# Kernel optimization log

Measured on AMD Instinct MI355X. Metric: run time of the kernel, lower is better.

The kernel has to match this reference:

```python
import jax, jax.numpy as jnp
import numpy as np
from jax import lax

# PRPN (Parse-Read-Predict Network), eval mode (all dropout off, BatchNorm in eval
# with running stats mean=0/var=1, rmask=ones). Submodule math follows the upstream
# yikangshen/PRPN implementation vendored by jiant: ParsingNetwork (conv gate stack,
# hard hardtanh memory gates with cumprod over slots), ReadingNetwork (masked-softmax
# attention over nslots memory + LayerNorm LSTM cell, shift-append memory update),
# PredictNetwork (attention over prediction memory, res=0 -> Linear+BN+Tanh head).

T, B, V, D, H, S, L, NL = 192, 32, 50000, 384, 384, 15, 5, 2
RES = 0.1
G4 = 4 * H
BN_SC = np.float32(1.0 / np.sqrt(1.0 + 1e-5))   # eval BatchNorm with mean=0, var=1
INV_SQRT_H = np.float32(1.0 / np.sqrt(H))


def _layer_norm(x, g, b, eps=1e-6):
    # torch-style LayerNorm with unbiased std (x.std(-1))
    mu = jnp.mean(x, -1, keepdims=True)
    var = jnp.sum((x - mu) ** 2, -1, keepdims=True) / (x.shape[-1] - 1)
    return g * (x - mu) / (jnp.sqrt(var) + eps) + b


def _msoftmax(logits, gate, eps=1e-8):
    # blocks.softmax: exp-normalize then multiply by (soft) gate mask before sum
    e = jnp.exp(logits - jnp.max(logits, -1, keepdims=True)) * gate
    return e / (jnp.sum(e, -1, keepdims=True) + eps)


def _forward(input_ids, emb_w, pconv1_w, pconv1_b, pbn_g, pbn_b, pconv2_w, pconv2_b,
             r_wih, r_bih, r_whh, r_bhh, r_lnih_g, r_lnih_b, r_lnhh_g, r_lnhh_b,
             r_lnc_g, r_lnc_b, r_proj_w, r_proj_b,
             p_proj_w, p_proj_b, p_ffd_w, p_ffd_b, p_bn_g, p_bn_b):
    emb = emb_w[input_ids]                                        # (T,B,D)

    # ---- ParsingNetwork ----
    x = jnp.concatenate([jnp.zeros((L, B, D), emb.dtype), emb], 0)  # (T+L,B,D), zero history
    xc = jnp.transpose(x, (1, 2, 0))                              # (B,D,T+L)
    h1 = lax.conv_general_dilated(xc, pconv1_w, (1,), 'VALID',
                                  dimension_numbers=('NCH', 'OIH', 'NCH'))
    h1 = h1 + pconv1_b[None, :, None]
    h1 = jax.nn.relu(pbn_g[None, :, None] * h1 * BN_SC + pbn_b[None, :, None])  # (B,H,T)
    half = H // 2
    # Conv1d(nhid, 2, 1, groups=2): channel 0 from first half, channel 1 from second
    gate = jax.nn.sigmoid(jnp.einsum('bct,c->bt', h1[:, :half], pconv2_w[0]) + pconv2_b[0])
    gate_next = jax.nn.sigmoid(jnp.einsum('bct,c->bt', h1[:, half:], pconv2_w[1]) + pconv2_b[1])
    cum = jnp.concatenate([jnp.full((B, S), 1e9, gate.dtype), gate], 1)  # init cum_gate = +inf
    gate_hat = jnp.stack([cum[:, S - k:S - k + T] for k in range(S)], 2)  # (B,T,S)

    def mem_gate(g):  # hard gates: (hardtanh((g-ghat)/res*2+1)+1)/2, cumprod over slots
        u = (jnp.clip((g[:, :, None] - gate_hat) / RES * 2.0 + 1.0, -1.0, 1.0) + 1.0) * 0.5
        return jnp.cumprod(u, axis=2)

    mg = jnp.transpose(mem_gate(gate), (1, 0, 2))                 # (T,B,S)
    mgn = jnp.transpose(mem_gate(gate_next), (1, 0, 2))           # (T,B,S)

    # ---- per-timestep Read / Predict-attention loop ----
    def step(carry, xs):
        mem_h, mem_c, pmem = carry       # (NL,B,S,H),(NL,B,S,H),(B,S,H)
        e_t, mg_t, mgn_t = xs
        h = e_t
        nh, nc = [], []
        for j in range(NL):
            mh, mc = mem_h[j], mem_c[j]
            key_j = jnp.concatenate([h, mh[:, -1]], -1) @ r_proj_w[j].T + r_proj_b[j]
            att = _msoftmax(jnp.einsum('bsh,bh->bs', mh, key_j) * INV_SQRT_H, mg_t)
            sel_h = jnp.einsum('bs,bsh->bh', att, mh)
            sel_c = jnp.einsum('bs,bsh->bh', att, mc)
            gates = (_layer_norm(h @ r_wih[j].T + r_bih[j], r_lnih_g[j], r_lnih_b[j])
                     + _layer_norm(sel_h @ r_whh[j].T + r_bhh[j], r_lnhh_g[j], r_lnhh_b[j]))
            i_g, f_g, c_g, o_g = jnp.split(gates, 4, axis=-1)
            c_new = jax.nn.sigmoid(f_g) * sel_c + jax.nn.sigmoid(i_g) * jnp.tanh(c_g)
            h_new = jax.nn.sigmoid(o_g) * jnp.tanh(_layer_norm(c_new, r_lnc_g[j], r_lnc_b[j]))
            nh.append(jnp.concatenate([mh[:, 1:], h_new[:, None]], 1))
            nc.append(jnp.concatenate([mc[:, 1:], c_new[:, None]], 1))
            h = h_new
        pkey = jnp.concatenate([h, pmem[:, -1]], -1) @ p_proj_w.T + p_proj_b
        patt = _msoftmax(jnp.einsum('bsh,bh->bs', pmem, pkey) * INV_SQRT_H, mgn_t)
        sel = jnp.einsum('bs,bsh->bh', patt, pmem)
        pmem_new = jnp.concatenate([pmem[:, 1:], h[:, None]], 1)
        return (jnp.stack(nh), jnp.stack(nc), pmem_new), (h, sel)

    carry0 = (jnp.zeros((NL, B, S, H), emb.dtype),
              jnp.zeros((NL, B, S, H), emb.dtype),
              jnp.zeros((B, S, H), emb.dtype))
    _, (out_h, out_sel) = lax.scan(step, carry0, (emb, mg, mgn))

    # ---- PredictNetwork head (res=0): Linear(2H->D) + BN(eval) + Tanh ----
    flat = jnp.concatenate([out_h.reshape(T * B, H), out_sel.reshape(T * B, H)], -1)
    y = flat @ p_ffd_w.T + p_ffd_b
    y = jnp.tanh(p_bn_g * y * BN_SC + p_bn_b)
    return y.reshape(T, B, D)


def setup_inputs() -> dict:
    key = jax.random.key(0)
    ks = iter(jax.random.split(key, 16))

    def rn(shape, s=0.05):
        return jax.random.normal(next(ks), shape, dtype=jnp.float32) * s

    return {
        "input_ids": jax.random.randint(next(ks), (T, B), 0, V),
        "emb_w": rn((V, D), 0.01),
        "pconv1_w": rn((H, D, L + 1)),
        "pconv1_b": jnp.zeros((H,), jnp.float32),
        "pbn_g": jnp.ones((H,), jnp.float32),
        "pbn_b": jnp.zeros((H,), jnp.float32),
        "pconv2_w": rn((2, H // 2)),
        "pconv2_b": jnp.zeros((2,), jnp.float32),
        "r_wih": rn((NL, G4, D)),
        "r_bih": jnp.zeros((NL, G4), jnp.float32),
        "r_whh": rn((NL, G4, H)),
        "r_bhh": jnp.zeros((NL, G4), jnp.float32),
        "r_lnih_g": jnp.ones((NL, G4), jnp.float32),
        "r_lnih_b": jnp.zeros((NL, G4), jnp.float32),
        "r_lnhh_g": jnp.ones((NL, G4), jnp.float32),
        "r_lnhh_b": jnp.zeros((NL, G4), jnp.float32),
        "r_lnc_g": jnp.ones((NL, H), jnp.float32),
        "r_lnc_b": jnp.zeros((NL, H), jnp.float32),
        "r_proj_w": rn((NL, H, D + H)),
        "r_proj_b": jnp.zeros((NL, H), jnp.float32),
        "p_proj_w": rn((H, 2 * H)),
        "p_proj_b": jnp.zeros((H,), jnp.float32),
        "p_ffd_w": rn((D, 2 * H)),
        "p_ffd_b": jnp.zeros((D,), jnp.float32),
        "p_bn_g": jnp.ones((D,), jnp.float32),
        "p_bn_b": jnp.zeros((D,), jnp.float32),
    }


def reference(input_ids, emb_w, pconv1_w, pconv1_b, pbn_g, pbn_b, pconv2_w, pconv2_b,
              r_wih, r_bih, r_whh, r_bhh, r_lnih_g, r_lnih_b, r_lnhh_g, r_lnhh_b,
              r_lnc_g, r_lnc_b, r_proj_w, r_proj_b,
              p_proj_w, p_proj_b, p_ffd_w, p_ffd_b, p_bn_g, p_bn_b):
    out = _forward(input_ids, emb_w, pconv1_w, pconv1_b, pbn_g, pbn_b, pconv2_w, pconv2_b,
                   r_wih, r_bih, r_whh, r_bhh, r_lnih_g, r_lnih_b, r_lnhh_g, r_lnhh_b,
                   r_lnc_g, r_lnc_b, r_proj_w, r_proj_b,
                   p_proj_w, p_proj_b, p_ffd_w, p_ffd_b, p_bn_g, p_bn_b)
    mask = input_ids != 0
    return out, mask
```

## Files before the change

kernel.cpp:

```cpp
#include <hip/hip_runtime.h>


#define TT 192
#define TB 6144

constexpr size_t O_EMB    = 0;
constexpr size_t O_IH0LN  = 2359296;
constexpr size_t O_KEY0E  = 11796480;
constexpr size_t O_MG     = 14155776;
constexpr size_t O_MGN    = 14247936;
constexpr size_t O_H1     = 14340096;
constexpr size_t O_GATEA  = 16699392;
constexpr size_t O_GATEB  = 16705536;
constexpr size_t O_OUTHS  = 16711680;
constexpr size_t O_MEMH0  = 21430272;
constexpr size_t O_MEMC0  = 21614592;
constexpr size_t O_MEMH1  = 21798912;
constexpr size_t O_MEMC1  = 21983232;
constexpr size_t O_PMEM   = 22167552;
constexpr size_t O_P0     = 22351872;
constexpr size_t O_P1     = 23089152;
constexpr size_t O_HNEW0  = 23826432;
constexpr size_t O_HNEW1  = 23838720;
constexpr size_t O_IH1RAW = 23851008;
constexpr size_t O_KEY1H  = 23900160;
constexpr size_t O_KEY0MH = 23912448;
constexpr size_t O_KEY1MH = 23924736;
constexpr size_t O_PKEYH  = 23937024;
constexpr size_t O_PKEYMH = 23949312;
constexpr size_t O_BAR    = 23973888;
constexpr size_t O_WSEND  = 23974176;

__device__ __forceinline__ float sigmoidf(float x) { return 1.f / (1.f + expf(-x)); }

__device__ __forceinline__ float ldx(const float* p) {
  return __hip_atomic_load(p, __ATOMIC_RELAXED, __HIP_MEMORY_SCOPE_AGENT);
}
__device__ __forceinline__ void stx(float* p, float v) {
  __hip_atomic_store(p, v, __ATOMIC_RELAXED, __HIP_MEMORY_SCOPE_AGENT);
}
__device__ __forceinline__ unsigned ldu(const unsigned* p) {
  return __hip_atomic_load(p, __ATOMIC_RELAXED, __HIP_MEMORY_SCOPE_AGENT);
}

constexpr float BN_SC = 0.9999950000374997f;
constexpr float INV_SQRT_H = 0.05103103630798288f;

__device__ __forceinline__ float blockSum(float v, float* red) {
#pragma unroll
  for (int off = 32; off > 0; off >>= 1) v += __shfl_down(v, off, 64);
  __syncthreads();
  if ((threadIdx.x & 63) == 0) red[threadIdx.x >> 6] = v;
  __syncthreads();
  return red[0] + red[1] + red[2] + red[3];
}

__global__ __launch_bounds__(256) void k_zero(float* p, int n) {
  int i = blockIdx.x * 256 + threadIdx.x;
  int stride = gridDim.x * 256;
  for (; i < n; i += stride) p[i] = 0.f;
}

__global__ __launch_bounds__(256) void k_emb(const int* ids, const float* emb_w,
                                             float* emb, float* out) {
  size_t idx = (size_t)blockIdx.x * 256 + threadIdx.x;
  size_t stride = (size_t)gridDim.x * 256;
  for (size_t i = idx; i < (size_t)TB * 384; i += stride) {
    size_t tb = i / 384, d = i - tb * 384;
    int id = ids[tb];
    emb[i] = emb_w[(size_t)id * 384 + d];
    if (i < TB) out[(size_t)TB * 384 + i] = (ids[i] != 0) ? 1.f : 0.f;
  }
}

__global__ __launch_bounds__(256) void k_conv(const float* emb, const float* W1, const float* cbias,
                                              const float* bng, const float* bnb, float* h1) {
  __shared__ float As[32][68];
  __shared__ float Bs[32][68];
  int n0 = blockIdx.x * 64, m0 = blockIdx.y * 64;
  int tid = threadIdx.x;
  float acc[4][4] = {};
  int mi = tid >> 3, kq = tid & 7;
  int ni = tid >> 2, kb = tid & 3;
  for (int kk = 0; kk < 2304; kk += 32) {
    int kc = kk / 384, dbase = kk - kc * 384;
    __syncthreads();
#pragma unroll
    for (int p = 0; p < 2; ++p) {
      int m = m0 + mi + 32 * p;
      int b = m / 192, t = m - b * 192;
      int tt = t + kc - 5;
      float4 v = {0.f, 0.f, 0.f, 0.f};
      if (tt >= 0) v = *(const float4*)(emb + ((size_t)tt * 32 + b) * 384 + dbase + kq * 4);
      As[kq * 4 + 0][mi + 32 * p] = v.x; As[kq * 4 + 1][mi + 32 * p] = v.y;
      As[kq * 4 + 2][mi + 32 * p] = v.z; As[kq * 4 + 3][mi + 32 * p] = v.w;
    }
#pragma unroll
    for (int i = 0; i < 8; ++i) {
      int d = dbase + kb * 8 + i;
      Bs[kb * 8 + i][ni] = W1[(size_t)(n0 + ni) * 2304 + d * 6 + kc];
    }
    __syncthreads();
    int ty = tid >> 4, tx = tid & 15;
#pragma unroll
    for (int k = 0; k < 32; ++k) {
      float4 a = *(const float4*)(&As[k][ty * 4]);
      float4 bv = *(const float4*)(&Bs[k][tx * 4]);
      acc[0][0] += a.x * bv.x; acc[0][1] += a.x * bv.y; acc[0][2] += a.x * bv.z; acc[0][3] += a.x * bv.w;
      acc[1][0] += a.y * bv.x; acc[1][1] += a.y * bv.y; acc[1][2] += a.y * bv.z; acc[1][3] += a.y * bv.w;
      acc[2][0] += a.z * bv.x; acc[2][1] += a.z * bv.y; acc[2][2] += a.z * bv.z; acc[2][3] += a.z * bv.w;
      acc[3][0] += a.w * bv.x; acc[3][1] += a.w * bv.y; acc[3][2] += a.w * bv.z; acc[3][3] += a.w * bv.w;
    }
  }
  int ty = tid >> 4, tx = tid & 15;
#pragma unroll
  for (int i = 0; i < 4; ++i) {
    int m = m0 + ty * 4 + i;
#pragma unroll
    for (int j = 0; j < 4; ++j) {
      int n = n0 + tx * 4 + j;
      float v = acc[i][j] + cbias[n];
      v = bng[n] * v * BN_SC + bnb[n];
      h1[(size_t)m * 384 + n] = fmaxf(v, 0.f);
    }
  }
}

__global__ __launch_bounds__(256) void k_gate(const float* h1, const float* w2, const float* b2,
                                              float* gA, float* gB) {
  __shared__ float red[8];
  int bt = blockIdx.x, tid = threadIdx.x;
  float v0 = 0.f, v1 = 0.f;
  if (tid < 192) {
    v0 = h1[(size_t)bt * 384 + tid] * w2[tid];
    v1 = h1[(size_t)bt * 384 + 192 + tid] * w2[192 + tid];
  }
  float s0 = blockSum(v0, red);
  float s1 = blockSum(v1, red);
  if (tid == 0) {
    gA[bt] = 1.f / (1.f + expf(-(s0 + b2[0])));
    gB[bt] = 1.f / (1.f + expf(-(s1 + b2[1])));
  }
}

__global__ __launch_bounds__(256) void k_mg(const float* gA, const float* gB, float* mg, float* mgn) {
  int idx = blockIdx.x * 256 + threadIdx.x;
  if (idx >= TB) return;
  int t = idx >> 5, b = idx & 31;
  float g = gA[b * 192 + t], gn = gB[b * 192 + t];
  float p = 1.f, pn = 1.f;
  for (int k = 0; k < 15; ++k) {
    float ghat = (k <= t) ? gA[b * 192 + t - k] : 1e9f;
    float u = fminf(fmaxf((g - ghat) / 0.1f * 2.f + 1.f, -1.f), 1.f);
    float un = fminf(fmaxf((gn - ghat) / 0.1f * 2.f + 1.f, -1.f), 1.f);
    p *= (u + 1.f) * 0.5f;
    pn *= (un + 1.f) * 0.5f;
    mg[(size_t)idx * 15 + k] = p;
    mgn[(size_t)idx * 15 + k] = pn;
  }
}

__global__ __launch_bounds__(256) void k_gemm(const float* A, int lda, const float* W, int ldw,
                                              const float* bias, float* Cf, int ldc, int K, int mode,
                                              const float* bng, const float* bnb, float* Cb) {
  __shared__ float As[32][68];
  __shared__ float Bs[32][68];
  int n0 = blockIdx.x * 64, m0 = blockIdx.y * 64;
  int tid = threadIdx.x;
  float acc[4][4] = {};
  int mi = tid >> 3, kq = tid & 7;
  int ni = tid >> 2, kb = tid & 3;
  for (int kk = 0; kk < K; kk += 32) {
    __syncthreads();
#pragma unroll
    for (int p = 0; p < 2; ++p) {
      int m = m0 + mi + 32 * p;
      float4 v = *(const float4*)(A + (size_t)m * lda + kk + kq * 4);
      As[kq * 4 + 0][mi + 32 * p] = v.x; As[kq * 4 + 1][mi + 32 * p] = v.y;
      As[kq * 4 + 2][mi + 32 * p] = v.z; As[kq * 4 + 3][mi + 32 * p] = v.w;
    }
    {
      const float* wp = W + (size_t)(n0 + ni) * ldw + kk + kb * 8;
      float4 q0 = *(const float4*)(wp);
      float4 q1 = *(const float4*)(wp + 4);
      Bs[kb * 8 + 0][ni] = q0.x; Bs[kb * 8 + 1][ni] = q0.y;
      Bs[kb * 8 + 2][ni] = q0.z; Bs[kb * 8 + 3][ni] = q0.w;
      Bs[kb * 8 + 4][ni] = q1.x; Bs[kb * 8 + 5][ni] = q1.y;
      Bs[kb * 8 + 6][ni] = q1.z; Bs[kb * 8 + 7][ni] = q1.w;
    }
    __syncthreads();
    int ty = tid >> 4, tx = tid & 15;
#pragma unroll
    for (int k = 0; k < 32; ++k) {
      float4 a = *(const float4*)(&As[k][ty * 4]);
      float4 bv = *(const float4*)(&Bs[k][tx * 4]);
      acc[0][0] += a.x * bv.x; acc[0][1] += a.x * bv.y; acc[0][2] += a.x * bv.z; acc[0][3] += a.x * bv.w;
      acc[1][0] += a.y * bv.x; acc[1][1] += a.y * bv.y; acc[1][2] += a.y * bv.z; acc[1][3] += a.y * bv.w;
      acc[2][0] += a.z * bv.x; acc[2][1] += a.z * bv.y; acc[2][2] += a.z * bv.z; acc[2][3] += a.z * bv.w;
      acc[3][0] += a.w * bv.x; acc[3][1] += a.w * bv.y; acc[3][2] += a.w * bv.z; acc[3][3] += a.w * bv.w;
    }
  }
  int ty = tid >> 4, tx = tid & 15;
#pragma unroll
  for (int i = 0; i < 4; ++i) {
    int m = m0 + ty * 4 + i;
#pragma unroll
    for (int j = 0; j < 4; ++j) {
      int n = n0 + tx * 4 + j;
      float v = acc[i][j];
      if (bias) v += bias[n];
      if (mode == 0) Cf[(size_t)m * ldc + n] = v;
      else Cb[(size_t)m * ldc + n] = tanhf(bng[n] * v * BN_SC + bnb[n]);
    }
  }
}

__global__ __launch_bounds__(256) void k_ln_rows(float* X, const float* g, const float* bt) {
  __shared__ float red[8];
  float* x = X + (size_t)blockIdx.x * 1536;
  int tid = threadIdx.x;
  float ps = 0.f;
  for (int i = tid; i < 1536; i += 256) ps += x[i];
  float mu = blockSum(ps, red) * (1.f / 1536.f);
  ps = 0.f;
  for (int i = tid; i < 1536; i += 256) { float d = x[i] - mu; ps += d * d; }
  float inv = 1.f / (sqrtf(blockSum(ps, red) * (1.f / 1535.f)) + 1e-6f);
  for (int i = tid; i < 1536; i += 256) x[i] = g[i] * (x[i] - mu) * inv + bt[i];
}

struct ScanArgs {
  float* ws;
  const float *r_whh, *r_bhh, *r_lnhh_g, *r_lnhh_b, *r_lnih_g, *r_lnih_b;
  const float *r_lnc_g, *r_lnc_b, *r_wih, *r_bih, *r_proj_w, *r_proj_b;
  const float *p_proj_w, *p_proj_b;
};

struct GJob { const float* W; int ldw; int koff; const float* bias; float* dst; int rstride; int ncols; };

__device__ __forceinline__ void resolveJob(const GJob* J, int col, const float*& W, int& ldw, int& koff,
                                           const float*& bias, float*& dst, int& rstride, int& cc) {
  int c = col;
#pragma unroll
  for (int j = 0; j < 4; ++j) {
    if (c < J[j].ncols) {
      W = J[j].W; ldw = J[j].ldw; koff = J[j].koff; bias = J[j].bias;
      dst = J[j].dst; rstride = J[j].rstride; cc = c; return;
    }
    c -= J[j].ncols;
  }
  W = J[0].W; ldw = J[0].ldw; koff = J[0].koff; bias = J[0].bias;
  dst = J[0].dst; rstride = J[0].rstride; cc = 0;
}

__device__ void grid_barrier(unsigned* bar, int wg, unsigned k) {
  __syncthreads();
  if (threadIdx.x == 0) {
    const int g = wg >> 4;
    unsigned arr = __hip_atomic_fetch_add(bar + g * 16, 1u, __ATOMIC_RELAXED, __HIP_MEMORY_SCOPE_AGENT);
    if (arr == k * 16u + 15u) {
      unsigned ra = __hip_atomic_fetch_add(bar + 128, 1u, __ATOMIC_RELAXED, __HIP_MEMORY_SCOPE_AGENT);
      if (ra == k * 8u + 7u) {
        __hip_atomic_store(bar + 144, k + 1u, __ATOMIC_RELAXED, __HIP_MEMORY_SCOPE_AGENT);
      } else {
        while (ldu(bar + 144) < k + 1u) __builtin_amdgcn_s_sleep(2);
      }
      __hip_atomic_store(bar + 160 + g * 16, k + 1u, __ATOMIC_RELAXED, __HIP_MEMORY_SCOPE_AGENT);
    } else {
      while (ldu(bar + 160 + g * 16) < k + 1u) __builtin_amdgcn_s_sleep(8);
    }
  }
  __syncthreads();
}

__device__ void gemm_phase(const float* src, const GJob* J, int NC, int gwg, float* red) {
  const int tid = threadIdx.x;
  const int b = tid & 31, cg = tid >> 5;
  const int colsPer = NC / 96;
  const int base = gwg * colsPer;
  const int k0 = cg * 48;
  float xr[48];
  const float* xp = src + b * 384 + k0;
#pragma unroll
  for (int q = 0; q < 48; ++q) xr[q] = ldx(xp + q);
#pragma unroll
  for (int ci = 0; ci < 28; ++ci) {
    if (ci >= colsPer) break;
    const float* W; int ldw, koff; const float* bias; float* dst; int rstride; int cc;
    resolveJob(J, base + ci, W, ldw, koff, bias, dst, rstride, cc);
    const float* wr = W + (size_t)cc * ldw + koff + k0;
    float a = 0.f;
#pragma unroll
    for (int q = 0; q < 12; ++q) {
      float4 w = *(const float4*)(wr + q * 4);
      a += w.x * xr[q * 4 + 0] + w.y * xr[q * 4 + 1]
         + w.z * xr[q * 4 + 2] + w.w * xr[q * 4 + 3];
    }
    red[(cg * colsPer + ci) * 32 + b] = a;
  }
  __syncthreads();
  const int pairs = colsPer * 32;
  for (int pi = tid; pi < pairs; pi += 256) {
    int bb = pi / colsPer, ci = pi - bb * colsPer;
    float s = 0.f;
#pragma unroll
    for (int g = 0; g < 8; ++g) s += red[(g * colsPer + ci) * 32 + bb];
    const float* W; int ldw, koff; const float* bias; float* dst; int rstride; int cc;
    resolveJob(J, base + ci, W, ldw, koff, bias, dst, rstride, cc);
    if (bias) s += bias[cc];
    stx(dst + (size_t)bb * rstride + cc, s);
  }
  __syncthreads();
}

__device__ void per_b_layer(int layer, int t, int b, const ScanArgs& A, float* sm) {
  float* ws = A.ws;
  const int tid = threadIdx.x;
  const size_t tb = (size_t)t * 32 + b;
  float* memh = ws + (layer ? O_MEMH1 : O_MEMH0) + (size_t)b * 15 * 384;
  float* memc = ws + (layer ? O_MEMC1 : O_MEMC0) + (size_t)b * 15 * 384;
  float* P = ws + (layer ? O_P1 : O_P0) + (size_t)b * 15 * 1536;
  float* keyl = sm; float* logit = sm + 384; float* att = sm + 400; float* red = sm + 416;
  float* ghh = sm + 448; float* gih = sm + 1984; float* selc = sm + 3520;
  float* cnew = sm + 3904; float* ogat = sm + 4288;

  for (int h = tid; h < 384; h += 256) {
    float k1, k2;
    if (layer == 0) { k1 = ws[O_KEY0E + tb * 384 + h]; k2 = ldx(ws + O_KEY0MH + (size_t)b * 384 + h); }
    else { k1 = ldx(ws + O_KEY1H + (size_t)b * 384 + h); k2 = ldx(ws + O_KEY1MH + (size_t)b * 384 + h); }
    keyl[h] = k1 + k2;
  }
  __syncthreads();
  {
    int s = tid >> 4, l = tid & 15;
    if (s < 15) {
      const float* mh = memh + ((t + s) % 15) * 384;
      float p = 0.f;
      for (int k = l; k < 384; k += 16) p += mh[k] * keyl[k];
      p += __shfl_down(p, 8, 64); p += __shfl_down(p, 4, 64);
      p += __shfl_down(p, 2, 64); p += __shfl_down(p, 1, 64);
      if (l == 0) logit[s] = p * INV_SQRT_H;
    }
  }
  __syncthreads();
  if (tid == 0) {
    const float* mgp = ws + O_MG + tb * 15;
    float m = logit[0];
    for (int i = 1; i < 15; ++i) m = fmaxf(m, logit[i]);
    float sum = 0.f;
    for (int i = 0; i < 15; ++i) { float e = expf(logit[i] - m) * mgp[i]; att[i] = e; sum += e; }
    float inv = 1.f / (sum + 1e-8f);
    for (int i = 0; i < 15; ++i) att[i] *= inv;
  }
  __syncthreads();
  float av[15]; int pidx[15];
#pragma unroll
  for (int i = 0; i < 15; ++i) { av[i] = att[i]; pidx[i] = (t + i) % 15; }
  const float* bhh = A.r_bhh + layer * 1536;
  for (int n = tid; n < 1536; n += 256) {
    float acc = bhh[n];
#pragma unroll
    for (int i = 0; i < 15; ++i) acc += av[i] * ldx(P + (size_t)pidx[i] * 1536 + n);
    ghh[n] = acc;
  }
  for (int h = tid; h < 384; h += 256) {
    float acc = 0.f;
#pragma unroll
    for (int i = 0; i < 15; ++i) acc += av[i] * memc[pidx[i] * 384 + h];
    selc[h] = acc;
  }
  if (layer) {
    for (int n = tid; n < 1536; n += 256) gih[n] = ldx(ws + O_IH1RAW + (size_t)b * 1536 + n);
  }
  __syncthreads();
  float ps = 0.f;
  for (int n = tid; n < 1536; n += 256) ps += ghh[n];
  float mu_hh = blockSum(ps, red) * (1.f / 1536.f);
  ps = 0.f;
  for (int n = tid; n < 1536; n += 256) { float d = ghh[n] - mu_hh; ps += d * d; }
  float inv_hh = 1.f / (sqrtf(blockSum(ps, red) * (1.f / 1535.f)) + 1e-6f);
  float mu_ih = 0.f, inv_ih = 0.f;
  if (layer) {
    ps = 0.f;
    for (int n = tid; n < 1536; n += 256) ps += gih[n];
    mu_ih = blockSum(ps, red) * (1.f / 1536.f);
    ps = 0.f;
    for (int n = tid; n < 1536; n += 256) { float d = gih[n] - mu_ih; ps += d * d; }
    inv_ih = 1.f / (sqrtf(blockSum(ps, red) * (1.f / 1535.f)) + 1e-6f);
  }
  const float *hg = A.r_lnhh_g + layer * 1536, *hb = A.r_lnhh_b + layer * 1536;
  const float *ig = A.r_lnih_g + 1536, *ib = A.r_lnih_b + 1536;
  for (int h = tid; h < 384; h += 256) {
    float gi, gf, gc, go;
    if (layer == 0) {
      const float* ihr = ws + O_IH0LN + tb * 1536;
      gi = ihr[h]; gf = ihr[384 + h]; gc = ihr[768 + h]; go = ihr[1152 + h];
    } else {
      gi = ig[h] * (gih[h] - mu_ih) * inv_ih + ib[h];
      gf = ig[384 + h] * (gih[384 + h] - mu_ih) * inv_ih + ib[384 + h];
      gc = ig[768 + h] * (gih[768 + h] - mu_ih) * inv_ih + ib[768 + h];
      go = ig[1152 + h] * (gih[1152 + h] - mu_ih) * inv_ih + ib[1152 + h];
    }
    gi += hg[h] * (ghh[h] - mu_hh) * inv_hh + hb[h];
    gf += hg[384 + h] * (ghh[384 + h] - mu_hh) * inv_hh + hb[384 + h];
    gc += hg[768 + h] * (ghh[768 + h] - mu_hh) * inv_hh + hb[768 + h];
    go += hg[1152 + h] * (ghh[1152 + h] - mu_hh) * inv_hh + hb[1152 + h];
    float c = sigmoidf(gf) * selc[h] + sigmoidf(gi) * tanhf(gc);
    cnew[h] = c; ogat[h] = go;
  }
  __syncthreads();
  ps = 0.f;
  for (int h = tid; h < 384; h += 256) ps += cnew[h];
  float mu_c = blockSum(ps, red) * (1.f / 384.f);
  ps = 0.f;
  for (int h = tid; h < 384; h += 256) { float d = cnew[h] - mu_c; ps += d * d; }
  float inv_c = 1.f / (sqrtf(blockSum(ps, red) * (1.f / 383.f)) + 1e-6f);
  const float *lcg = A.r_lnc_g + layer * 384, *lcb = A.r_lnc_b + layer * 384;
  const int slot = t % 15;
  for (int h = tid; h < 384; h += 256) {
    float hn = sigmoidf(ogat[h]) * tanhf(lcg[h] * (cnew[h] - mu_c) * inv_c + lcb[h]);
    memh[slot * 384 + h] = hn;
    memc[slot * 384 + h] = cnew[h];
    if (layer == 0) stx(ws + O_HNEW0 + (size_t)b * 384 + h, hn);
    else { stx(ws + O_HNEW1 + (size_t)b * 384 + h, hn); ws[O_OUTHS + tb * 768 + h] = hn; }
  }
}

__device__ void per_b_predict(int tau, int b, const ScanArgs& A, float* sm) {
  float* ws = A.ws;
  const int tid = threadIdx.x;
  const size_t tb = (size_t)tau * 32 + b;
  float* pmem = ws + O_PMEM + (size_t)b * 15 * 384;
  float* keyl = sm; float* logit = sm + 384; float* att = sm + 400;
  for (int h = tid; h < 384; h += 256)
    keyl[h] = ldx(ws + O_PKEYH + (size_t)b * 384 + h)
            + ldx(ws + O_PKEYMH + (size_t)(tau & 1) * 12288 + (size_t)b * 384 + h);
  __syncthreads();
  {
    int s = tid >> 4, l = tid & 15;
    if (s < 15) {
      const float* mh = pmem + ((tau + s) % 15) * 384;
      float p = 0.f;
      for (int k = l; k < 384; k += 16) p += mh[k] * keyl[k];
      p += __shfl_down(p, 8, 64); p += __shfl_down(p, 4, 64);
      p += __shfl_down(p, 2, 64); p += __shfl_down(p, 1, 64);
      if (l == 0) logit[s] = p * INV_SQRT_H;
    }
  }
  __syncthreads();
  if (tid == 0) {
    const float* mgp = ws + O_MGN + tb * 15;
    float m = logit[0];
    for (int i = 1; i < 15; ++i) m = fmaxf(m, logit[i]);
    float sum = 0.f;
    for (int i = 0; i < 15; ++i) { float e = expf(logit[i] - m) * mgp[i]; att[i] = e; sum += e; }
    float inv = 1.f / (sum + 1e-8f);
    for (int i = 0; i < 15; ++i) att[i] *= inv;
  }
  __syncthreads();
  float av[15]; int pidx[15];
#pragma unroll
  for (int i = 0; i < 15; ++i) { av[i] = att[i]; pidx[i] = (tau + i) % 15; }
  for (int h = tid; h < 384; h += 256) {
    float acc = 0.f;
#pragma unroll
    for (int i = 0; i < 15; ++i) acc += av[i] * pmem[pidx[i] * 384 + h];
    ws[O_OUTHS + tb * 768 + 384 + h] = acc;
  }
  __syncthreads();
  for (int h = tid; h < 384; h += 256)
    pmem[(tau % 15) * 384 + h] = ldx(ws + O_HNEW1 + (size_t)b * 384 + h);
}

__global__ __launch_bounds__(256) void k_scan(ScanArgs A) {
  __shared__ float sm[7424];
  float* ws = A.ws;
  unsigned* bar = (unsigned*)(ws + O_BAR);
  const int wg = blockIdx.x;
  unsigned bk = 0;
  for (int t = 0; t <= TT; ++t) {
    if (wg < 32) {
      if (t < TT) per_b_layer(0, t, wg, A, sm);
    } else {
      GJob J[4] = {
        { A.r_whh + 589824, 384, 0, nullptr, ws + O_P1 + (size_t)((t + 14) % 15) * 1536, 23040, 1536 },
        { A.r_proj_w + 294912, 768, 384, nullptr, ws + O_KEY1MH, 384, 384 },
        { A.p_proj_w, 768, 0, A.p_proj_b, ws + O_PKEYH, 384, 384 },
        { A.p_proj_w, 768, 384, nullptr, ws + O_PKEYMH + (size_t)(t & 1) * 12288, 384, 384 },
      };
      gemm_phase(ws + O_HNEW1, J, 2688, wg - 32, sm);
    }
    grid_barrier(bar, wg, bk); ++bk;
    if (wg < 32) {
      if (t >= 1) per_b_predict(t - 1, wg, A, sm);
    } else if (t < TT) {
      GJob J[4] = {
        { A.r_wih + 589824, 384, 0, A.r_bih + 1536, ws + O_IH1RAW, 1536, 1536 },
        { A.r_proj_w + 294912, 768, 0, A.r_proj_b + 384, ws + O_KEY1H, 384, 384 },
        { nullptr, 0, 0, nullptr, nullptr, 0, 0 },
        { nullptr, 0, 0, nullptr, nullptr, 0, 0 },
      };
      gemm_phase(ws + O_HNEW0, J, 1920, wg - 32, sm);
    }
    if (t == TT) break;
    grid_barrier(bar, wg, bk); ++bk;
    if (wg < 32) {
      per_b_layer(1, t, wg, A, sm);
    } else {
      GJob J[4] = {
        { A.r_whh, 384, 0, nullptr, ws + O_P0 + (size_t)(t % 15) * 1536, 23040, 1536 },
        { A.r_proj_w, 768, 384, nullptr, ws + O_KEY0MH, 384, 384 },
        { nullptr, 0, 0, nullptr, nullptr, 0, 0 },
        { nullptr, 0, 0, nullptr, nullptr, 0, 0 },
      };
      gemm_phase(ws + O_HNEW0, J, 1920, wg - 32, sm);
    }
    grid_barrier(bar, wg, bk); ++bk;
  }
}

extern "C" void kernel_launch(void* const* d_in, const int* in_sizes, int n_in,
                              void* d_out, int out_size, void* d_ws, size_t ws_size,
                              hipStream_t stream) {
  const int* ids = (const int*)d_in[0];
  const float* emb_w = (const float*)d_in[1];
  const float* pconv1_w = (const float*)d_in[2];
  const float* pconv1_b = (const float*)d_in[3];
  const float* pbn_g = (const float*)d_in[4];
  const float* pbn_b = (const float*)d_in[5];
  const float* pconv2_w = (const float*)d_in[6];
  const float* pconv2_b = (const float*)d_in[7];
  const float* r_wih = (const float*)d_in[8];
  const float* r_bih = (const float*)d_in[9];
  const float* r_whh = (const float*)d_in[10];
  const float* r_bhh = (const float*)d_in[11];
  const float* r_lnih_g = (const float*)d_in[12];
  const float* r_lnih_b = (const float*)d_in[13];
  const float* r_lnhh_g = (const float*)d_in[14];
  const float* r_lnhh_b = (const float*)d_in[15];
  const float* r_lnc_g = (const float*)d_in[16];
  const float* r_lnc_b = (const float*)d_in[17];
  const float* r_proj_w = (const float*)d_in[18];
  const float* r_proj_b = (const float*)d_in[19];
  const float* p_proj_w = (const float*)d_in[20];
  const float* p_proj_b = (const float*)d_in[21];
  const float* p_ffd_w = (const float*)d_in[22];
  const float* p_ffd_b = (const float*)d_in[23];
  const float* p_bn_g = (const float*)d_in[24];
  const float* p_bn_b = (const float*)d_in[25];
  float* ws = (float*)d_ws;
  float* out = (float*)d_out;

  k_zero<<<1024, 256, 0, stream>>>(ws + O_MEMH0, (int)(O_WSEND - O_MEMH0));
  k_emb<<<4096, 256, 0, stream>>>(ids, emb_w, ws + O_EMB, out);
  k_conv<<<dim3(6, 96), 256, 0, stream>>>(ws + O_EMB, pconv1_w, pconv1_b, pbn_g, pbn_b, ws + O_H1);
  k_gate<<<6144, 256, 0, stream>>>(ws + O_H1, pconv2_w, pconv2_b, ws + O_GATEA, ws + O_GATEB);
  k_mg<<<24, 256, 0, stream>>>(ws + O_GATEA, ws + O_GATEB, ws + O_MG, ws + O_MGN);
  k_gemm<<<dim3(24, 96), 256, 0, stream>>>(ws + O_EMB, 384, r_wih, 384, r_bih,
                                           ws + O_IH0LN, 1536, 384, 0, nullptr, nullptr, nullptr);
  k_gemm<<<dim3(6, 96), 256, 0, stream>>>(ws + O_EMB, 384, r_proj_w, 768, r_proj_b,
                                          ws + O_KEY0E, 384, 384, 0, nullptr, nullptr, nullptr);
  k_ln_rows<<<6144, 256, 0, stream>>>(ws + O_IH0LN, r_lnih_g, r_lnih_b);
  ScanArgs SA{ws, r_whh, r_bhh, r_lnhh_g, r_lnhh_b, r_lnih_g, r_lnih_b,
              r_lnc_g, r_lnc_b, r_wih, r_bih, r_proj_w, r_proj_b, p_proj_w, p_proj_b};
  k_scan<<<128, 256, 0, stream>>>(SA);
  k_gemm<<<dim3(6, 96), 256, 0, stream>>>(ws + O_OUTHS, 768, p_ffd_w, 768, p_ffd_b,
                                          nullptr, 384, 768, 1, p_bn_g, p_bn_b, out);
}
```

Before: 15.15 ms.

## Spread scan GEMV phases over more workgroups with shared-memory staged inputs

Launches the persistent scan kernel with 256 workgroups instead of 128, so the GEMV phases use 224 workgroups instead of 96, each covering a smaller column range. The grid barrier is widened to 16 groups to match. Each GEMV workgroup now stages the full hidden-state input into padded shared memory before computing, and the reduction buffer is padded to avoid bank conflicts. This cuts per-workgroup serial work on the recurrent critical path, at the cost of more barrier participants, more LDS per workgroup, and possibly more than one workgroup per CU.

```diff
diff --git a/kernel.cpp b/kernel.cpp
--- a/kernel.cpp
+++ b/kernel.cpp
@@ -29,7 +29,7 @@
 constexpr size_t O_PKEYH  = 23937024;
 constexpr size_t O_PKEYMH = 23949312;
 constexpr size_t O_BAR    = 23973888;
-constexpr size_t O_WSEND  = 23974176;
+constexpr size_t O_WSEND  = 23974432;
 
 __device__ __forceinline__ float sigmoidf(float x) { return 1.f / (1.f + expf(-x)); }
 
@@ -258,35 +258,42 @@
     const int g = wg >> 4;
     unsigned arr = __hip_atomic_fetch_add(bar + g * 16, 1u, __ATOMIC_RELAXED, __HIP_MEMORY_SCOPE_AGENT);
     if (arr == k * 16u + 15u) {
-      unsigned ra = __hip_atomic_fetch_add(bar + 128, 1u, __ATOMIC_RELAXED, __HIP_MEMORY_SCOPE_AGENT);
-      if (ra == k * 8u + 7u) {
-        __hip_atomic_store(bar + 144, k + 1u, __ATOMIC_RELAXED, __HIP_MEMORY_SCOPE_AGENT);
+      unsigned ra = __hip_atomic_fetch_add(bar + 256, 1u, __ATOMIC_RELAXED, __HIP_MEMORY_SCOPE_AGENT);
+      if (ra == k * 16u + 15u) {
+        __hip_atomic_store(bar + 272, k + 1u, __ATOMIC_RELAXED, __HIP_MEMORY_SCOPE_AGENT);
       } else {
-        while (ldu(bar + 144) < k + 1u) __builtin_amdgcn_s_sleep(2);
+        while (ldu(bar + 272) < k + 1u) __builtin_amdgcn_s_sleep(2);
       }
-      __hip_atomic_store(bar + 160 + g * 16, k + 1u, __ATOMIC_RELAXED, __HIP_MEMORY_SCOPE_AGENT);
+      __hip_atomic_store(bar + 288 + g * 16, k + 1u, __ATOMIC_RELAXED, __HIP_MEMORY_SCOPE_AGENT);
     } else {
-      while (ldu(bar + 160 + g * 16) < k + 1u) __builtin_amdgcn_s_sleep(8);
-    }
-  }
-  __syncthreads();
-}
-
-__device__ void gemm_phase(const float* src, const GJob* J, int NC, int gwg, float* red) {
+      while (ldu(bar + 288 + g * 16) < k + 1u) __builtin_amdgcn_s_sleep(8);
+    }
+  }
+  __syncthreads();
+}
+
+#define NG_GEMV 224
+__device__ void gemm_phase(const float* src, const GJob* J, int NC, int gwg,
+                           float* xs , float* red ) {
   const int tid = threadIdx.x;
+  for (int j = tid; j < 12288; j += 256) {
+    int bb = j >> 8;
+    bb = j / 384;
+    int kk = j - bb * 384;
+    xs[bb * 385 + kk] = ldx(src + j);
+  }
+  __syncthreads();
   const int b = tid & 31, cg = tid >> 5;
-  const int colsPer = NC / 96;
-  const int base = gwg * colsPer;
+  const int c0 = (gwg * NC) / NG_GEMV, c1 = ((gwg + 1) * NC) / NG_GEMV;
+  const int colsPer = c1 - c0;
   const int k0 = cg * 48;
   float xr[48];
-  const float* xp = src + b * 384 + k0;
-#pragma unroll
-  for (int q = 0; q < 48; ++q) xr[q] = ldx(xp + q);
-#pragma unroll
-  for (int ci = 0; ci < 28; ++ci) {
-    if (ci >= colsPer) break;
+  const float* xp = xs + b * 385 + k0;
+#pragma unroll
+  for (int q = 0; q < 48; ++q) xr[q] = xp[q];
+  for (int ci = 0; ci < colsPer; ++ci) {
     const float* W; int ldw, koff; const float* bias; float* dst; int rstride; int cc;
-    resolveJob(J, base + ci, W, ldw, koff, bias, dst, rstride, cc);
+    resolveJob(J, c0 + ci, W, ldw, koff, bias, dst, rstride, cc);
     const float* wr = W + (size_t)cc * ldw + koff + k0;
     float a = 0.f;
 #pragma unroll
@@ -295,7 +302,7 @@
       a += w.x * xr[q * 4 + 0] + w.y * xr[q * 4 + 1]
          + w.z * xr[q * 4 + 2] + w.w * xr[q * 4 + 3];
     }
-    red[(cg * colsPer + ci) * 32 + b] = a;
+    red[(cg * colsPer + ci) * 33 + b] = a;
   }
   __syncthreads();
   const int pairs = colsPer * 32;
@@ -303,9 +310,9 @@
     int bb = pi / colsPer, ci = pi - bb * colsPer;
     float s = 0.f;
 #pragma unroll
-    for (int g = 0; g < 8; ++g) s += red[(g * colsPer + ci) * 32 + bb];
+    for (int g = 0; g < 8; ++g) s += red[(g * colsPer + ci) * 33 + bb];
     const float* W; int ldw, koff; const float* bias; float* dst; int rstride; int cc;
-    resolveJob(J, base + ci, W, ldw, koff, bias, dst, rstride, cc);
+    resolveJob(J, c0 + ci, W, ldw, koff, bias, dst, rstride, cc);
     if (bias) s += bias[cc];
     stx(dst + (size_t)bb * rstride + cc, s);
   }
@@ -472,10 +479,12 @@
 }
 
 __global__ __launch_bounds__(256) void k_scan(ScanArgs A) {
-  __shared__ float sm[7424];
+  __shared__ float sm[16032];
   float* ws = A.ws;
   unsigned* bar = (unsigned*)(ws + O_BAR);
   const int wg = blockIdx.x;
+  float* xs = sm;
+  float* red = sm + 12320;
   unsigned bk = 0;
   for (int t = 0; t <= TT; ++t) {
     if (wg < 32) {
@@ -487,7 +496,7 @@
         { A.p_proj_w, 768, 0, A.p_proj_b, ws + O_PKEYH, 384, 384 },
         { A.p_proj_w, 768, 384, nullptr, ws + O_PKEYMH + (size_t)(t & 1) * 12288, 384, 384 },
       };
-      gemm_phase(ws + O_HNEW1, J, 2688, wg - 32, sm);
+      gemm_phase(ws + O_HNEW1, J, 2688, wg - 32, xs, red);
     }
     grid_barrier(bar, wg, bk); ++bk;
     if (wg < 32) {
@@ -499,7 +508,7 @@
         { nullptr, 0, 0, nullptr, nullptr, 0, 0 },
         { nullptr, 0, 0, nullptr, nullptr, 0, 0 },
       };
-      gemm_phase(ws + O_HNEW0, J, 1920, wg - 32, sm);
+      gemm_phase(ws + O_HNEW0, J, 1920, wg - 32, xs, red);
     }
     if (t == TT) break;
     grid_barrier(bar, wg, bk); ++bk;
@@ -512,7 +521,7 @@
         { nullptr, 0, 0, nullptr, nullptr, 0, 0 },
         { nullptr, 0, 0, nullptr, nullptr, 0, 0 },
       };
-      gemm_phase(ws + O_HNEW0, J, 1920, wg - 32, sm);
+      gemm_phase(ws + O_HNEW0, J, 1920, wg - 32, xs, red);
     }
     grid_barrier(bar, wg, bk); ++bk;
   }
@@ -562,7 +571,7 @@
   k_ln_rows<<<6144, 256, 0, stream>>>(ws + O_IH0LN, r_lnih_g, r_lnih_b);
   ScanArgs SA{ws, r_whh, r_bhh, r_lnhh_g, r_lnhh_b, r_lnih_g, r_lnih_b,
               r_lnc_g, r_lnc_b, r_wih, r_bih, r_proj_w, r_proj_b, p_proj_w, p_proj_b};
-  k_scan<<<128, 256, 0, stream>>>(SA);
+  k_scan<<<256, 256, 0, stream>>>(SA);
   k_gemm<<<dim3(6, 96), 256, 0, stream>>>(ws + O_OUTHS, 768, p_ffd_w, 768, p_ffd_b,
                                           nullptr, 384, 768, 1, p_bn_g, p_bn_b, out);
 }
```

Result: faster. 14.27 ms (-5.8%).
